# Kernel optimization log

Measured on AMD Instinct MI355X. Metric: run time of the kernel, lower is better.

## Reference

```python
import jax, jax.numpy as jnp
import numpy as np

NUM_CLASSES = 80
TOPK = 100
EPS = 1e-6


def _conv(x, w, b, pad):
    y = jax.lax.conv_general_dilated(
        x, w, window_strides=(1, 1), padding=[(pad, pad), (pad, pad)],
        dimension_numbers=('NCHW', 'OIHW', 'NCHW'))
    return y + b[None, :, None, None]


def _seek_local_maximum(p):
    # 8-neighbor local-maximum test with zero padding, plus >= EPS threshold.
    pp = jnp.pad(p, ((0, 0), (0, 0), (1, 1), (1, 1)))
    m = ((p >= pp[:, :, :-2, 1:-1]) & (p >= pp[:, :, 2:, 1:-1]) &
         (p >= pp[:, :, 1:-1, :-2]) & (p >= pp[:, :, 1:-1, 2:]) &
         (p >= pp[:, :, :-2, :-2]) & (p >= pp[:, :, :-2, 2:]) &
         (p >= pp[:, :, 2:, :-2]) & (p >= pp[:, :, 2:, 2:]) &
         (p >= EPS))
    return m.astype(p.dtype)


def setup_inputs() -> dict:
    key = jax.random.key(0)
    k = jax.random.split(key, 4)
    B, C, H, W = 8, 256, 128, 128
    return {
        'x': jax.random.normal(k[0], (B, C, H, W), jnp.float32),
        'pos_embeddings': jax.random.normal(k[1], (1, C, H, W), jnp.float32),
        'w1': jax.random.normal(k[2], (C, C, 3, 3), jnp.float32) * 0.02,
        'b1': jnp.zeros((C,), jnp.float32),
        'w2': jax.random.normal(k[3], (NUM_CLASSES + 1, C, 1, 1), jnp.float32) * 0.02,
        'b2': jnp.zeros((NUM_CLASSES + 1,), jnp.float32),
    }


def reference(x, pos_embeddings, w1, b1, w2, b2):
    b, c, h, w = x.shape
    # conv3x3 -> relu -> conv1x1 class logits  [b, num_classes+1, h, w]
    logits = _conv(jax.nn.relu(_conv(x, w1, b1, 1)), w2, b2, 0)
    probs = jax.nn.softmax(logits, axis=1)
    # keep only the winning foreground class per pixel (one-hot mask)
    cls_idx = jnp.argmax(probs[:, :NUM_CLASSES], axis=1)  # [b, h, w]
    one_hot = jax.nn.one_hot(cls_idx, NUM_CLASSES + 1, dtype=probs.dtype)
    probs = probs * jnp.transpose(one_hot, (0, 3, 1, 2))
    # boost local maxima (unrolled NMS) then topk over best-class score map
    probs = probs + _seek_local_maximum(probs)
    scores = jnp.max(probs[:, :NUM_CLASSES], axis=1).reshape(b, h * w)
    _, idx = jax.lax.top_k(scores, TOPK)  # [b, TOPK]
    topk_proposals = jnp.take_along_axis(
        x.reshape(b, c, h * w), idx[:, None, :], axis=2)
    pe = jnp.broadcast_to(pos_embeddings, (b,) + pos_embeddings.shape[1:])
    topk_pos_embeddings = jnp.take_along_axis(
        pe.reshape(b, -1, h * w), idx[:, None, :], axis=2)
    # eval mode: topk_locations is None in the original; omit it here
    return topk_proposals, topk_pos_embeddings, logits
```

## Files before the change

### kernel.cpp

```cpp
#include <hip/hip_runtime.h>
#include <cmath>

#define BATCH 8
#define CHN 256
#define HH 128
#define WW 128
#define HWSZ (HH*WW)
#define NCLS 81
#define NFG 80
#define KTOP 100
#define EPSV 1e-6f

typedef __attribute__((ext_vector_type(8))) short short8;
typedef __attribute__((ext_vector_type(4))) float f32x4;

__device__ __forceinline__ ushort f2bf(float f) {
    unsigned u = __float_as_uint(f);
    return (ushort)((u + 0x7FFFu + ((u >> 16) & 1u)) >> 16);
}
__device__ __forceinline__ float bf2f(ushort h) {
    return __uint_as_float(((unsigned)h) << 16);
}

__device__ __forceinline__ void gl16(const void* g, void* l) {
    __builtin_amdgcn_global_load_lds(
        (const __attribute__((address_space(1))) void*)g,
        (__attribute__((address_space(3))) void*)l, 16, 0, 0);
}

__global__ __launch_bounds__(256) void prep_x(
    const float* __restrict__ x, ushort* __restrict__ xh, ushort* __restrict__ xl)
{
    __shared__ float tile[32 * 321];
    const int blk = blockIdx.x;
    const int q4 = blk & 3, h = (blk >> 2) & 127, b = blk >> 9;
    const int w0 = q4 << 5;
    const int t = threadIdx.x;
    const int px1 = t & 31, cq = t >> 5;

    const float* xb = x + ((size_t)b * CHN) * HWSZ + h * WW + w0;
#pragma unroll 4
    for (int i = 0; i < 32; ++i) {
        tile[px1 * 321 + i * 10 + cq] = xb[(size_t)(i * 8 + cq) * HWSZ + px1];
    }
    __syncthreads();
    for (int i = 0; i < 4; ++i) {
        int u = i * 256 + t;
        int c8 = u & 31, px = u >> 5;
        short8 hv, lv;
#pragma unroll
        for (int j = 0; j < 8; ++j) {
            float f = tile[px * 321 + c8 * 10 + j];
            ushort hb = f2bf(f);
            hv[j] = (short)hb;
            lv[j] = (short)f2bf(f - bf2f(hb));
        }
        size_t addr = ((size_t)b * HWSZ + h * WW + w0 + px) * CHN + c8 * 8;
        *(short8*)(xh + addr) = hv;
        *(short8*)(xl + addr) = lv;
    }
}

__global__ __launch_bounds__(256) void prep_w(
    const float* __restrict__ w1, const float* __restrict__ w2,
    ushort* __restrict__ Bsw, ushort* __restrict__ w2sw)
{
    int i = blockIdx.x * 256 + threadIdx.x;
    if (i < 73728) {
        int tap  = i >> 13;
        int rem  = i & 8191;
        int kt   = rem >> 10;
        int rem2 = rem & 1023;
        int ntg  = rem2 >> 6;
        int lane = rem2 & 63;
        int oc   = ntg * 16 + (lane & 15);
        int ic0  = kt * 32 + (lane >> 4) * 8;
        size_t base = (size_t)(tap * 8 + kt) * 16384 + (size_t)ntg * 512 + lane * 8;
#pragma unroll
        for (int j = 0; j < 8; ++j) {
            float w  = w1[(size_t)oc * 2304 + (ic0 + j) * 9 + tap];
            ushort hb = f2bf(w);
            Bsw[base + j]        = hb;
            Bsw[base + 8192 + j] = f2bf(w - bf2f(hb));
        }
    } else {
        int j2 = i - 73728;
        int kt   = j2 / 768;
        int rem  = j2 - kt * 768;
        int spl  = rem / 384;
        int rem2 = rem - spl * 384;
        int ntg  = rem2 >> 6;
        int lane = rem2 & 63;
        int oc   = ntg * 16 + (lane & 15);
        int ic0  = kt * 32 + (lane >> 4) * 8;
        size_t base = (size_t)(kt * 12 + spl * 6 + ntg) * 512 + lane * 8;
#pragma unroll
        for (int j = 0; j < 8; ++j) {
            float w = (oc < NCLS) ? w2[(size_t)oc * CHN + ic0 + j] : 0.f;
            ushort hb = f2bf(w);
            w2sw[base + j] = spl ? f2bf(w - bf2f(hb)) : hb;
        }
    }
}

__global__ __launch_bounds__(256, 2) void conv3_pipe(
    const ushort* __restrict__ xh, const ushort* __restrict__ xl,
    const ushort* __restrict__ Bsw, const float* __restrict__ b1,
    float* __restrict__ y)
{
    __shared__ ushort A[3][2][132 * 32];

    const int blk  = blockIdx.x;
    const int b    = blk & 7;
    const int h    = blk >> 3;
    const int t    = threadIdx.x;
    const int lane = t & 63;
    const int w    = t >> 6;
    const int l15  = lane & 15;
    const int q    = lane >> 4;

    int colb[4], basew[4];
#pragma unroll
    for (int r = 0; r < 4; ++r) {
        int e   = (r * 256 + t) & 511;
        int pxs = (e >> 2) + 1;
        int qq  = e & 3;
        int qs  = qq ^ ((pxs >> 1) & 3);
        colb[r]  = (pxs - 1) * CHN + qs * 8;
        basew[r] = ((((r * 256 + (t & 192)) & 511) >> 2) + 1) * 32;
    }

    int abase[3];
#pragma unroll
    for (int kw = 0; kw < 3; ++kw) {
        int p0 = l15 + kw;
        abase[kw] = p0 * 64 + ((q ^ ((p0 >> 1) & 3)) << 4);
    }

    const short8 zz = {0, 0, 0, 0, 0, 0, 0, 0};
    f32x4 acc[8][4];
#pragma unroll
    for (int i = 0; i < 8; ++i)
#pragma unroll
        for (int j = 0; j < 4; ++j) { f32x4 z = {0.f, 0.f, 0.f, 0.f}; acc[i][j] = z; }

    if (t < 96) {
        int sl = t >> 5, rr = t & 31, arr = rr >> 4, pp = (rr >> 2) & 3, qq = rr & 3;
        int pxs = pp ? 128 + pp : 0;
        *(short8*)&A[sl][arr][pxs * 32 + qq * 8] = zz;
    }
    if (h == 0 || h == 127) {
        const int sl = (h == 0) ? 0 : 2;
        for (int u = t; u < 1056; u += 256) {
            int arr = u >= 528; int v = arr ? u - 528 : u;
            *(short8*)&A[sl][arr][v * 8] = zz;
        }
    }

    auto stage = [&](int sn) {
        int kt1 = sn / 3;
        int kh1 = sn - kt1 * 3;
        int gh  = h - 1 + kh1;
        if ((unsigned)gh < (unsigned)HH) {
            size_t rowb = ((size_t)(b * HH + gh) * WW) * CHN + kt1 * 32;
#pragma unroll
            for (int r = 0; r < 4; ++r) {
                const ushort* g = (r < 2 ? xh : xl) + rowb + colb[r];
                gl16(g, &A[kh1][r >> 1][basew[r]]);
            }
        }
    };

    stage(0);
    stage(1);

#pragma unroll 1
    for (int s = 0; s < 24; ++s) {
        const int kt = s / 3;
        const int kh = s - kt * 3;
        {
            const int kh1n = (s + 1) % 3;
            const bool nx4 = (s < 23) &&
                !((h == 0 && kh1n == 0) || (h == 127 && kh1n == 2));
            if (nx4) asm volatile("s_waitcnt vmcnt(4) lgkmcnt(0)" ::: "memory");
            else     asm volatile("s_waitcnt vmcnt(0) lgkmcnt(0)" ::: "memory");
            __builtin_amdgcn_s_barrier();
            __builtin_amdgcn_sched_barrier(0);
        }
#pragma unroll
        for (int kw = 0; kw < 3; ++kw) {
            const int tap = kh * 3 + kw;
            const char* bkh = (const char*)Bsw +
                ((size_t)(tap * 8 + kt) << 15) + (w << 12) + (lane << 4);
            const char* bkl = bkh + 16384;
            short8 bh[4], bl[4];
#pragma unroll
            for (int nt = 0; nt < 4; ++nt) {
                bh[nt] = *(const short8*)(bkh + nt * 1024);
                bl[nt] = *(const short8*)(bkl + nt * 1024);
            }
            if (kw == 0 && s < 22) stage(s + 2);
            const char* pah = (const char*)&A[kh][0][0] + abase[kw];
            const char* pal = (const char*)&A[kh][1][0] + abase[kw];
#pragma unroll
            for (int mth = 0; mth < 8; mth += 4) {
                short8 ahf[4], alf[4];
#pragma unroll
                for (int mm = 0; mm < 4; ++mm) {
                    ahf[mm] = *(const short8*)(pah + (mth + mm) * 1024);
                    alf[mm] = *(const short8*)(pal + (mth + mm) * 1024);
                }
                __builtin_amdgcn_s_setprio(1);
#pragma unroll
                for (int nt = 0; nt < 4; ++nt) {
#pragma unroll
                    for (int mm = 0; mm < 4; ++mm)
                        acc[mth + mm][nt] = __builtin_amdgcn_mfma_f32_16x16x32_bf16(
                            ahf[mm], bh[nt], acc[mth + mm][nt], 0, 0, 0);
#pragma unroll
                    for (int mm = 0; mm < 4; ++mm)
                        acc[mth + mm][nt] = __builtin_amdgcn_mfma_f32_16x16x32_bf16(
                            ahf[mm], bl[nt], acc[mth + mm][nt], 0, 0, 0);
#pragma unroll
                    for (int mm = 0; mm < 4; ++mm)
                        acc[mth + mm][nt] = __builtin_amdgcn_mfma_f32_16x16x32_bf16(
                            alf[mm], bh[nt], acc[mth + mm][nt], 0, 0, 0);
                }
                __builtin_amdgcn_s_setprio(0);
            }
        }
    }

    const size_t rowbase = (size_t)b * HWSZ + h * WW;
#pragma unroll
    for (int nt = 0; nt < 4; ++nt) {
        const int oc = w * 64 + nt * 16 + l15;
        const float bias = b1[oc];
#pragma unroll
        for (int mt = 0; mt < 8; ++mt) {
#pragma unroll
            for (int r = 0; r < 4; ++r) {
                const int px = mt * 16 + q * 4 + r;
                float v = acc[mt][nt][r] + bias;
                y[(rowbase + px) * CHN + oc] = v > 0.f ? v : 0.f;
            }
        }
    }
}

__global__ __launch_bounds__(256) void head_mfma(
    const float* __restrict__ y, const ushort* __restrict__ w2sw,
    const float* __restrict__ b2, float* __restrict__ logits_out,
    int* __restrict__ cls_map, float* __restrict__ prob_map)
{
    __shared__ float ls[128][97];
    const int blk = blockIdx.x;
    const int b = blk >> 7, h = blk & 127;
    const int t = threadIdx.x, lane = t & 63, wm = t >> 6;
    const int l15 = lane & 15, q = lane >> 4;

    f32x4 acc[2][6];
#pragma unroll
    for (int i = 0; i < 2; ++i)
#pragma unroll
        for (int j = 0; j < 6; ++j) { f32x4 z = {0.f, 0.f, 0.f, 0.f}; acc[i][j] = z; }

    const size_t rowbase = (size_t)b * HWSZ + h * WW;
    const float* yb0 = y + (rowbase + wm * 32 + l15) * CHN + q * 8;
    const float* yb1 = yb0 + 16 * CHN;

    float4 fa[2][4], fb[2][4];
#pragma unroll
    for (int k = 0; k < 4; ++k) {
        fa[0][k] = *(const float4*)(yb0 + k * 32);
        fb[0][k] = *(const float4*)(yb0 + k * 32 + 4);
        fa[1][k] = *(const float4*)(yb1 + k * 32);
        fb[1][k] = *(const float4*)(yb1 + k * 32 + 4);
    }

#pragma unroll
    for (int kt = 0; kt < 8; ++kt) {
        const int sl = kt & 3;
        short8 ah[2], al[2];
#pragma unroll
        for (int mt = 0; mt < 2; ++mt) {
            float4 f0 = fa[mt][sl];
            float4 f1 = fb[mt][sl];
            float fv[8] = {f0.x, f0.y, f0.z, f0.w, f1.x, f1.y, f1.z, f1.w};
#pragma unroll
            for (int j = 0; j < 8; ++j) {
                ushort hb = f2bf(fv[j]);
                ah[mt][j] = (short)hb;
                al[mt][j] = (short)f2bf(fv[j] - bf2f(hb));
            }
        }
        if (kt < 4) {
            fa[0][sl] = *(const float4*)(yb0 + (kt + 4) * 32);
            fb[0][sl] = *(const float4*)(yb0 + (kt + 4) * 32 + 4);
            fa[1][sl] = *(const float4*)(yb1 + (kt + 4) * 32);
            fb[1][sl] = *(const float4*)(yb1 + (kt + 4) * 32 + 4);
        }
        const ushort* bk = w2sw + (size_t)kt * 12 * 512 + lane * 8;
#pragma unroll
        for (int nt = 0; nt < 6; ++nt) {
            short8 bh = *(const short8*)(bk + nt * 512);
            short8 bl = *(const short8*)(bk + (6 + nt) * 512);
#pragma unroll
            for (int mt = 0; mt < 2; ++mt) {
                acc[mt][nt] = __builtin_amdgcn_mfma_f32_16x16x32_bf16(ah[mt], bh, acc[mt][nt], 0, 0, 0);
                acc[mt][nt] = __builtin_amdgcn_mfma_f32_16x16x32_bf16(ah[mt], bl, acc[mt][nt], 0, 0, 0);
                acc[mt][nt] = __builtin_amdgcn_mfma_f32_16x16x32_bf16(al[mt], bh, acc[mt][nt], 0, 0, 0);
            }
        }
    }

#pragma unroll
    for (int nt = 0; nt < 6; ++nt) {
        const int oc = nt * 16 + l15;
        const float bias = (oc < NCLS) ? b2[oc] : 0.f;
#pragma unroll
        for (int mt = 0; mt < 2; ++mt) {
#pragma unroll
            for (int r = 0; r < 4; ++r) {
                const int px = wm * 32 + mt * 16 + q * 4 + r;
                ls[px][oc] = acc[mt][nt][r] + bias;
            }
        }
    }
    __syncthreads();

    for (int i = t; i < NCLS * 128; i += 256) {
        int c = i >> 7, px = i & 127;
        logits_out[((size_t)b * NCLS + c) * HWSZ + h * WW + px] = ls[px][c];
    }

    if (t < 128) {
        const int px = t;
        float m = -1e30f;
#pragma unroll
        for (int c = 0; c < NCLS; ++c) m = fmaxf(m, ls[px][c]);
        float s = 0.f;
        for (int c = 0; c < NCLS; ++c) s += expf(ls[px][c] - m);
        float best = -1e30f; int bc = 0;
        for (int c = 0; c < NFG; ++c) {
            float v = ls[px][c];
            if (v > best) { best = v; bc = c; }
        }
        cls_map[rowbase + px]  = bc;
        prob_map[rowbase + px] = expf(best - m) / s;
    }
}

__global__ __launch_bounds__(256) void locmax_kernel(
    const int* __restrict__ cls_map, const float* __restrict__ prob_map,
    float* __restrict__ score)
{
    int i = blockIdx.x * 256 + threadIdx.x;
    int b = i >> 14;
    int p = i & (HWSZ - 1);
    int h = p >> 7, w = p & 127;
    int mycls = cls_map[i];
    float myp = prob_map[i];
    bool lm = (myp >= EPSV);
#pragma unroll
    for (int dh = -1; dh <= 1; ++dh)
#pragma unroll
        for (int dw = -1; dw <= 1; ++dw) {
            if (dh == 0 && dw == 0) continue;
            int nh = h + dh, nw = w + dw;
            if ((unsigned)nh < HH && (unsigned)nw < WW) {
                int ni = b * HWSZ + nh * WW + nw;
                if (cls_map[ni] == mycls && myp < prob_map[ni]) lm = false;
            }
        }
    score[i] = myp + (lm ? 1.f : 0.f);
}

__global__ __launch_bounds__(1024) void topk_kernel(
    const float* __restrict__ score, int* __restrict__ idx_out)
{
    __shared__ unsigned int hist[256];
    __shared__ unsigned int suf[256];
    __shared__ unsigned long long cand[2048];
    __shared__ unsigned int sprefix, sneed, scntA, scntB;
    const int b = blockIdx.x;
    const int t = threadIdx.x;
    const float* sc = score + b * HWSZ;

    unsigned keys[16];
#pragma unroll
    for (int i = 0; i < 16; ++i)
        keys[i] = __float_as_uint(sc[t + (i << 10)]);

    if (t == 0) { sneed = KTOP; sprefix = 0; scntA = 0; scntB = 0; }

    for (int lvl = 0; lvl < 4; ++lvl) {
        const int shift = 24 - 8 * lvl;
        if (t < 256) hist[t] = 0;
        __syncthreads();
        const unsigned pref = sprefix;
#pragma unroll
        for (int i = 0; i < 16; ++i) {
            unsigned k = keys[i];
            bool match = (lvl == 0) || ((k >> (shift + 8)) == pref);
            if (match) atomicAdd(&hist[(k >> shift) & 255u], 1u);
        }
        __syncthreads();
        if (t < 256) suf[t] = hist[t];
        __syncthreads();
#pragma unroll
        for (int st = 1; st < 256; st <<= 1) {
            unsigned v = 0;
            if (t < 256 && t + st < 256) v = suf[t + st];
            __syncthreads();
            if (t < 256) suf[t] += v;
            __syncthreads();
        }
        const unsigned needv = sneed;
        __syncthreads();
        if (t < 256) {
            unsigned sj  = suf[t];
            unsigned sj1 = (t == 255) ? 0u : suf[t + 1];
            if (sj >= needv && sj1 < needv) {
                sprefix = (pref << 8) | (unsigned)t;
                sneed   = needv - sj1;
            }
        }
        __syncthreads();
    }

    const unsigned K = sprefix;
#pragma unroll
    for (int i = 0; i < 16; ++i) {
        unsigned k = keys[i];
        int p = t + (i << 10);
        if (k > K) {
            unsigned pos = atomicAdd(&scntA, 1u);
            cand[pos] = ((unsigned long long)k << 32) | (unsigned)(~p);
        } else if (k == K) {
            unsigned pos = atomicAdd(&scntB, 1u);
            if (pos < 1920u)
                cand[128 + pos] = ((unsigned long long)k << 32) | (unsigned)(~p);
        }
    }
    __syncthreads();
    const int cA = (int)scntA;
    const int cB = (int)(scntB < 1920u ? scntB : 1920u);
    const int Ctot = cA + cB;
    for (int ti = t; ti < Ctot; ti += 1024) {
        unsigned long long my = cand[ti < cA ? ti : 128 + (ti - cA)];
        int rank = 0;
        for (int j = 0; j < Ctot; ++j) {
            unsigned long long o = cand[j < cA ? j : 128 + (j - cA)];
            rank += (o > my) ? 1 : 0;
        }
        if (rank < KTOP)
            idx_out[b * KTOP + rank] =
                (int)(~(unsigned)(my & 0xFFFFFFFFull)) & (HWSZ - 1);
    }
}

__global__ __launch_bounds__(128) void gather_kernel(
    const float* __restrict__ x, const float* __restrict__ pos,
    const int* __restrict__ idx, float* __restrict__ out0,
    float* __restrict__ out1)
{
    int blk = blockIdx.x;
    int b = blk >> 8, c = blk & 255;
    int j = threadIdx.x;
    if (j < KTOP) {
        int pix = idx[b * KTOP + j];
        out0[((size_t)b * CHN + c) * KTOP + j] = x[((size_t)b * CHN + c) * HWSZ + pix];
        out1[((size_t)b * CHN + c) * KTOP + j] = pos[(size_t)c * HWSZ + pix];
    }
}

extern "C" void kernel_launch(void* const* d_in, const int* in_sizes, int n_in,
                              void* d_out, int out_size, void* d_ws, size_t ws_size,
                              hipStream_t stream) {
    (void)in_sizes; (void)n_in; (void)out_size; (void)ws_size;
    const float* x   = (const float*)d_in[0];
    const float* pos = (const float*)d_in[1];
    const float* w1  = (const float*)d_in[2];
    const float* b1  = (const float*)d_in[3];
    const float* w2  = (const float*)d_in[4];
    const float* b2  = (const float*)d_in[5];

    float* out0   = (float*)d_out;
    float* out1   = out0 + BATCH * CHN * KTOP;
    float* logits = out1 + BATCH * CHN * KTOP;

    char* ws = (char*)d_ws;
    const size_t NPX = (size_t)BATCH * HWSZ;

    size_t off = 0;
    int*    cls_map  = (int*)(ws + off);    off += NPX * 4;
    float*  prob_map = (float*)(ws + off);  off += NPX * 4;
    float*  score    = (float*)(ws + off);  off += NPX * 4;
    int*    idx      = (int*)(ws + off);    off += 4096;
    ushort* w2sw     = (ushort*)(ws + off); off += (size_t)8 * 12 * 512 * 2;
    ushort* Bsw      = (ushort*)(ws + off); off += (size_t)9 * 8 * 16384 * 2;
    ushort* xh       = (ushort*)(ws + off); off += NPX * CHN * 2;
    ushort* xl       = (ushort*)(ws + off); off += NPX * CHN * 2;
    float*  y        = (float*)(ws + off);  off += NPX * CHN * 4;

    prep_x<<<4096, 256, 0, stream>>>(x, xh, xl);
    prep_w<<<312, 256, 0, stream>>>(w1, w2, Bsw, w2sw);
    conv3_pipe<<<1024, 256, 0, stream>>>(xh, xl, Bsw, b1, y);
    head_mfma<<<1024, 256, 0, stream>>>(y, w2sw, b2, logits, cls_map, prob_map);
    locmax_kernel<<<(int)(NPX / 256), 256, 0, stream>>>(cls_map, prob_map, score);
    topk_kernel<<<BATCH, 1024, 0, stream>>>(score, idx);
    gather_kernel<<<BATCH * CHN, 128, 0, stream>>>(x, pos, idx, out0, out1);
}
```

Baseline: 664.4 us.

## Switch conv3x3 MFMA from 16x16x32 to 32x32x16 bf16 tiles

Changes the conv3x3 kernel's inner product from 16x16x32 MFMA instructions to 32x32x16 ones. It reorganizes the weight swizzle in prep_w, the LDS A-fragment addressing and the accumulator layout to match. The larger tiles mean fewer LDS fragment loads per FLOP and fewer MFMA issues, which should raise matrix-core utilisation. The epilogue's pixel-index mapping is rewritten for the 32x32 output layout, so any mistake there would show up as a correctness bug.

```diff
diff --git a/kernel.cpp b/kernel.cpp
--- a/kernel.cpp
+++ b/kernel.cpp
@@ -13,6 +13,7 @@
 
 typedef __attribute__((ext_vector_type(8))) short short8;
 typedef __attribute__((ext_vector_type(4))) float f32x4;
+typedef __attribute__((ext_vector_type(16))) float f32x16;
 
 __device__ __forceinline__ ushort f2bf(float f) {
     unsigned u = __float_as_uint(f);
@@ -71,11 +72,14 @@
         int rem  = i & 8191;
         int kt   = rem >> 10;
         int rem2 = rem & 1023;
-        int ntg  = rem2 >> 6;
+        int fgrp = rem2 >> 6;
         int lane = rem2 & 63;
-        int oc   = ntg * 16 + (lane & 15);
-        int ic0  = kt * 32 + (lane >> 4) * 8;
-        size_t base = (size_t)(tap * 8 + kt) * 16384 + (size_t)ntg * 512 + lane * 8;
+        int wv   = fgrp >> 2;
+        int n    = (fgrp >> 1) & 1;
+        int ks   = fgrp & 1;
+        int oc   = wv * 64 + n * 32 + (lane & 31);
+        int ic0  = kt * 32 + ks * 16 + (lane >> 5) * 8;
+        size_t base = (size_t)(tap * 8 + kt) * 16384 + (size_t)fgrp * 512 + lane * 8;
 #pragma unroll
         for (int j = 0; j < 8; ++j) {
             float w  = w1[(size_t)oc * 2304 + (ic0 + j) * 9 + tap];
@@ -116,8 +120,8 @@
     const int t    = threadIdx.x;
     const int lane = t & 63;
     const int w    = t >> 6;
-    const int l15  = lane & 15;
-    const int q    = lane >> 4;
+    const int la   = lane & 31;
+    const int g    = lane >> 5;
 
     int colb[4], basew[4];
 #pragma unroll
@@ -130,19 +134,24 @@
         basew[r] = ((((r * 256 + (t & 192)) & 511) >> 2) + 1) * 32;
     }
 
-    int abase[3];
+    int abks[3][2];
 #pragma unroll
     for (int kw = 0; kw < 3; ++kw) {
-        int p0 = l15 + kw;
-        abase[kw] = p0 * 64 + ((q ^ ((p0 >> 1) & 3)) << 4);
+        int la2 = la + kw;
+        int sw  = (la2 >> 1) & 3;
+#pragma unroll
+        for (int ks = 0; ks < 2; ++ks)
+            abks[kw][ks] = la2 * 64 + (((((ks << 1) | g)) ^ sw) << 4);
     }
 
     const short8 zz = {0, 0, 0, 0, 0, 0, 0, 0};
-    f32x4 acc[8][4];
-#pragma unroll
-    for (int i = 0; i < 8; ++i)
-#pragma unroll
-        for (int j = 0; j < 4; ++j) { f32x4 z = {0.f, 0.f, 0.f, 0.f}; acc[i][j] = z; }
+    f32x16 acc[4][2];
+#pragma unroll
+    for (int i = 0; i < 4; ++i)
+#pragma unroll
+        for (int j = 0; j < 2; ++j)
+#pragma unroll
+            for (int r = 0; r < 16; ++r) acc[i][j][r] = 0.f;
 
     if (t < 96) {
         int sl = t >> 5, rr = t & 31, arr = rr >> 4, pp = (rr >> 2) & 3, qq = rr & 3;
@@ -165,8 +174,8 @@
             size_t rowb = ((size_t)(b * HH + gh) * WW) * CHN + kt1 * 32;
 #pragma unroll
             for (int r = 0; r < 4; ++r) {
-                const ushort* g = (r < 2 ? xh : xl) + rowb + colb[r];
-                gl16(g, &A[kh1][r >> 1][basew[r]]);
+                const ushort* gp = (r < 2 ? xh : xl) + rowb + colb[r];
+                gl16(gp, &A[kh1][r >> 1][basew[r]]);
             }
         }
     };
@@ -193,39 +202,44 @@
             const char* bkh = (const char*)Bsw +
                 ((size_t)(tap * 8 + kt) << 15) + (w << 12) + (lane << 4);
             const char* bkl = bkh + 16384;
-            short8 bh[4], bl[4];
-#pragma unroll
-            for (int nt = 0; nt < 4; ++nt) {
-                bh[nt] = *(const short8*)(bkh + nt * 1024);
-                bl[nt] = *(const short8*)(bkl + nt * 1024);
-            }
+            short8 bh[2][2], bl[2][2];
+#pragma unroll
+            for (int n = 0; n < 2; ++n)
+#pragma unroll
+                for (int ks = 0; ks < 2; ++ks) {
+                    bh[n][ks] = *(const short8*)(bkh + (n * 2 + ks) * 1024);
+                    bl[n][ks] = *(const short8*)(bkl + (n * 2 + ks) * 1024);
+                }
             if (kw == 0 && s < 22) stage(s + 2);
-            const char* pah = (const char*)&A[kh][0][0] + abase[kw];
-            const char* pal = (const char*)&A[kh][1][0] + abase[kw];
-#pragma unroll
-            for (int mth = 0; mth < 8; mth += 4) {
-                short8 ahf[4], alf[4];
-#pragma unroll
-                for (int mm = 0; mm < 4; ++mm) {
-                    ahf[mm] = *(const short8*)(pah + (mth + mm) * 1024);
-                    alf[mm] = *(const short8*)(pal + (mth + mm) * 1024);
+            const char* pah = (const char*)&A[kh][0][0];
+            const char* pal = (const char*)&A[kh][1][0];
+#pragma unroll
+            for (int ks = 0; ks < 2; ++ks) {
+                short8 ah[4], al[4];
+#pragma unroll
+                for (int m = 0; m < 4; ++m) {
+                    ah[m] = *(const short8*)(pah + abks[kw][ks] + m * 2048);
+                    al[m] = *(const short8*)(pal + abks[kw][ks] + m * 2048);
                 }
                 __builtin_amdgcn_s_setprio(1);
 #pragma unroll
-                for (int nt = 0; nt < 4; ++nt) {
-#pragma unroll
-                    for (int mm = 0; mm < 4; ++mm)
-                        acc[mth + mm][nt] = __builtin_amdgcn_mfma_f32_16x16x32_bf16(
-                            ahf[mm], bh[nt], acc[mth + mm][nt], 0, 0, 0);
-#pragma unroll
-                    for (int mm = 0; mm < 4; ++mm)
-                        acc[mth + mm][nt] = __builtin_amdgcn_mfma_f32_16x16x32_bf16(
-                            ahf[mm], bl[nt], acc[mth + mm][nt], 0, 0, 0);
-#pragma unroll
-                    for (int mm = 0; mm < 4; ++mm)
-                        acc[mth + mm][nt] = __builtin_amdgcn_mfma_f32_16x16x32_bf16(
-                            alf[mm], bh[nt], acc[mth + mm][nt], 0, 0, 0);
-                }
+                for (int n = 0; n < 2; ++n)
+#pragma unroll
+                    for (int m = 0; m < 4; ++m)
+                        acc[m][n] = __builtin_amdgcn_mfma_f32_32x32x16_bf16(
+                            ah[m], bh[n][ks], acc[m][n], 0, 0, 0);
+#pragma unroll
+                for (int n = 0; n < 2; ++n)
+#pragma unroll
+                    for (int m = 0; m < 4; ++m)
+                        acc[m][n] = __builtin_amdgcn_mfma_f32_32x32x16_bf16(
+                            ah[m], bl[n][ks], acc[m][n], 0, 0, 0);
+#pragma unroll
+                for (int n = 0; n < 2; ++n)
+#pragma unroll
+                    for (int m = 0; m < 4; ++m)
+                        acc[m][n] = __builtin_amdgcn_mfma_f32_32x32x16_bf16(
+                            al[m], bh[n][ks], acc[m][n], 0, 0, 0);
                 __builtin_amdgcn_s_setprio(0);
             }
         }
@@ -233,15 +247,15 @@
 
     const size_t rowbase = (size_t)b * HWSZ + h * WW;
 #pragma unroll
-    for (int nt = 0; nt < 4; ++nt) {
-        const int oc = w * 64 + nt * 16 + l15;
+    for (int n = 0; n < 2; ++n) {
+        const int oc = w * 64 + n * 32 + la;
         const float bias = b1[oc];
 #pragma unroll
-        for (int mt = 0; mt < 8; ++mt) {
-#pragma unroll
-            for (int r = 0; r < 4; ++r) {
-                const int px = mt * 16 + q * 4 + r;
-                float v = acc[mt][nt][r] + bias;
+        for (int m = 0; m < 4; ++m) {
+#pragma unroll
+            for (int reg = 0; reg < 16; ++reg) {
+                const int px = m * 32 + (reg & 3) + 8 * (reg >> 2) + 4 * g;
+                float v = acc[m][n][reg] + bias;
                 y[(rowbase + px) * CHN + oc] = v > 0.f ? v : 0.f;
             }
         }
```

New measurement: 706.2 us. 6.3% more time.

## Split conv3x3 row tile into half-width blocks for higher occupancy

Applied to the files above, without the earlier changes.

The 3x3 conv kernel now processes 64 pixels of a row per block instead of 128, doubling the grid to 2048 blocks and halving both the accumulator register tile and the LDS staging buffer (with halo columns loaded separately). Launch bounds are raised to 3 blocks per SM to hide latency with more resident waves. In exchange, each B-weight fragment loaded from global memory is reused over half as many MFMAs, doubling weight traffic, and halo loads add some overhead.

```diff
diff --git a/kernel.cpp b/kernel.cpp
--- a/kernel.cpp
+++ b/kernel.cpp
@@ -103,32 +103,34 @@
     }
 }
 
-__global__ __launch_bounds__(256, 2) void conv3_pipe(
+__global__ __launch_bounds__(256, 3) void conv3_occ(
     const ushort* __restrict__ xh, const ushort* __restrict__ xl,
     const ushort* __restrict__ Bsw, const float* __restrict__ b1,
     float* __restrict__ y)
 {
-    __shared__ ushort A[3][2][132 * 32];
+    __shared__ ushort A[3][2][68 * 32];
 
     const int blk  = blockIdx.x;
     const int b    = blk & 7;
-    const int h    = blk >> 3;
+    const int h    = (blk >> 3) & 127;
+    const int ws2  = blk >> 10;
+    const int w0   = ws2 << 6;
     const int t    = threadIdx.x;
     const int lane = t & 63;
-    const int w    = t >> 6;
+    const int wv   = t >> 6;
     const int l15  = lane & 15;
     const int q    = lane >> 4;
 
-    int colb[4], basew[4];
-#pragma unroll
-    for (int r = 0; r < 4; ++r) {
-        int e   = (r * 256 + t) & 511;
-        int pxs = (e >> 2) + 1;
-        int qq  = e & 3;
-        int qs  = qq ^ ((pxs >> 1) & 3);
-        colb[r]  = (pxs - 1) * CHN + qs * 8;
-        basew[r] = ((((r * 256 + (t & 192)) & 511) >> 2) + 1) * 32;
-    }
+    const int mrow = 1 + wv * 16 + (lane >> 2);
+    const int mqs  = (lane & 3) ^ ((mrow >> 1) & 3);
+    const int mcol = (w0 + wv * 16 + (lane >> 2)) * CHN + mqs * 8;
+    const int mdst = (1 + wv * 16) * 32;
+    const int hrow = ws2 ? 0 : 65;
+    const int hgw  = w0 - 1 + hrow;
+    const int ha   = wv >> 1;
+    const int hqb  = (wv & 1) * 2;
+    const int hcol = hgw * CHN + (hqb + (lane & 1)) * 8;
+    const int hdst = hrow * 32 + hqb * 8;
 
     int abase[3];
 #pragma unroll
@@ -138,22 +140,22 @@
     }
 
     const short8 zz = {0, 0, 0, 0, 0, 0, 0, 0};
-    f32x4 acc[8][4];
-#pragma unroll
-    for (int i = 0; i < 8; ++i)
+    f32x4 acc[4][4];
+#pragma unroll
+    for (int i = 0; i < 4; ++i)
 #pragma unroll
         for (int j = 0; j < 4; ++j) { f32x4 z = {0.f, 0.f, 0.f, 0.f}; acc[i][j] = z; }
 
-    if (t < 96) {
-        int sl = t >> 5, rr = t & 31, arr = rr >> 4, pp = (rr >> 2) & 3, qq = rr & 3;
-        int pxs = pp ? 128 + pp : 0;
-        *(short8*)&A[sl][arr][pxs * 32 + qq * 8] = zz;
+    if (t < 24) {
+        int sl = t >> 3, rr = t & 7, a = rr >> 2, qq = rr & 3;
+        int zrow = ws2 ? 65 : 0;
+        *(short8*)&A[sl][a][zrow * 32 + qq * 8] = zz;
     }
     if (h == 0 || h == 127) {
         const int sl = (h == 0) ? 0 : 2;
-        for (int u = t; u < 1056; u += 256) {
-            int arr = u >= 528; int v = arr ? u - 528 : u;
-            *(short8*)&A[sl][arr][v * 8] = zz;
+        for (int u = t; u < 544; u += 256) {
+            int a = u >= 272; int v = a ? u - 272 : u;
+            *(short8*)&A[sl][a][v * 8] = zz;
         }
     }
 
@@ -163,11 +165,10 @@
         int gh  = h - 1 + kh1;
         if ((unsigned)gh < (unsigned)HH) {
             size_t rowb = ((size_t)(b * HH + gh) * WW) * CHN + kt1 * 32;
-#pragma unroll
-            for (int r = 0; r < 4; ++r) {
-                const ushort* g = (r < 2 ? xh : xl) + rowb + colb[r];
-                gl16(g, &A[kh1][r >> 1][basew[r]]);
-            }
+            gl16(xh + rowb + mcol, &A[kh1][0][mdst]);
+            gl16(xl + rowb + mcol, &A[kh1][1][mdst]);
+            if (lane < 2)
+                gl16((ha ? xl : xh) + rowb + hcol, &A[kh1][ha][hdst]);
         }
     };
 
@@ -180,10 +181,10 @@
         const int kh = s - kt * 3;
         {
             const int kh1n = (s + 1) % 3;
-            const bool nx4 = (s < 23) &&
+            const bool nx = (s < 23) &&
                 !((h == 0 && kh1n == 0) || (h == 127 && kh1n == 2));
-            if (nx4) asm volatile("s_waitcnt vmcnt(4) lgkmcnt(0)" ::: "memory");
-            else     asm volatile("s_waitcnt vmcnt(0) lgkmcnt(0)" ::: "memory");
+            if (nx) asm volatile("s_waitcnt vmcnt(3) lgkmcnt(0)" ::: "memory");
+            else    asm volatile("s_waitcnt vmcnt(0) lgkmcnt(0)" ::: "memory");
             __builtin_amdgcn_s_barrier();
             __builtin_amdgcn_sched_barrier(0);
         }
@@ -191,7 +192,7 @@
         for (int kw = 0; kw < 3; ++kw) {
             const int tap = kh * 3 + kw;
             const char* bkh = (const char*)Bsw +
-                ((size_t)(tap * 8 + kt) << 15) + (w << 12) + (lane << 4);
+                ((size_t)(tap * 8 + kt) << 15) + (wv << 12) + (lane << 4);
             const char* bkl = bkh + 16384;
             short8 bh[4], bl[4];
 #pragma unroll
@@ -201,43 +202,43 @@
             }
             if (kw == 0 && s < 22) stage(s + 2);
             const char* pah = (const char*)&A[kh][0][0] + abase[kw];
-            const char* pal = (const char*)&A[kh][1][0] + abase[kw];
-#pragma unroll
-            for (int mth = 0; mth < 8; mth += 4) {
-                short8 ahf[4], alf[4];
-#pragma unroll
-                for (int mm = 0; mm < 4; ++mm) {
-                    ahf[mm] = *(const short8*)(pah + (mth + mm) * 1024);
-                    alf[mm] = *(const short8*)(pal + (mth + mm) * 1024);
-                }
-                __builtin_amdgcn_s_setprio(1);
-#pragma unroll
-                for (int nt = 0; nt < 4; ++nt) {
-#pragma unroll
-                    for (int mm = 0; mm < 4; ++mm)
-                        acc[mth + mm][nt] = __builtin_amdgcn_mfma_f32_16x16x32_bf16(
-                            ahf[mm], bh[nt], acc[mth + mm][nt], 0, 0, 0);
-#pragma unroll
-                    for (int mm = 0; mm < 4; ++mm)
-                        acc[mth + mm][nt] = __builtin_amdgcn_mfma_f32_16x16x32_bf16(
-                            ahf[mm], bl[nt], acc[mth + mm][nt], 0, 0, 0);
-#pragma unroll
-                    for (int mm = 0; mm < 4; ++mm)
-                        acc[mth + mm][nt] = __builtin_amdgcn_mfma_f32_16x16x32_bf16(
-                            alf[mm], bh[nt], acc[mth + mm][nt], 0, 0, 0);
-                }
-                __builtin_amdgcn_s_setprio(0);
-            }
-        }
-    }
-
-    const size_t rowbase = (size_t)b * HWSZ + h * WW;
+            const char* pal = pah + 4352;
+            short8 ahf[4], alf[4];
+#pragma unroll
+            for (int mm = 0; mm < 4; ++mm) {
+                ahf[mm] = *(const short8*)(pah + mm * 1024);
+                alf[mm] = *(const short8*)(pal + mm * 1024);
+            }
+            __builtin_amdgcn_s_setprio(1);
+#pragma unroll
+            for (int nt = 0; nt < 4; ++nt)
+#pragma unroll
+                for (int mm = 0; mm < 4; ++mm)
+                    acc[mm][nt] = __builtin_amdgcn_mfma_f32_16x16x32_bf16(
+                        ahf[mm], bh[nt], acc[mm][nt], 0, 0, 0);
+#pragma unroll
+            for (int nt = 0; nt < 4; ++nt)
+#pragma unroll
+                for (int mm = 0; mm < 4; ++mm)
+                    acc[mm][nt] = __builtin_amdgcn_mfma_f32_16x16x32_bf16(
+                        ahf[mm], bl[nt], acc[mm][nt], 0, 0, 0);
+#pragma unroll
+            for (int nt = 0; nt < 4; ++nt)
+#pragma unroll
+                for (int mm = 0; mm < 4; ++mm)
+                    acc[mm][nt] = __builtin_amdgcn_mfma_f32_16x16x32_bf16(
+                        alf[mm], bh[nt], acc[mm][nt], 0, 0, 0);
+            __builtin_amdgcn_s_setprio(0);
+        }
+    }
+
+    const size_t rowbase = (size_t)b * HWSZ + h * WW + w0;
 #pragma unroll
     for (int nt = 0; nt < 4; ++nt) {
-        const int oc = w * 64 + nt * 16 + l15;
+        const int oc = wv * 64 + nt * 16 + l15;
         const float bias = b1[oc];
 #pragma unroll
-        for (int mt = 0; mt < 8; ++mt) {
+        for (int mt = 0; mt < 4; ++mt) {
 #pragma unroll
             for (int r = 0; r < 4; ++r) {
                 const int px = mt * 16 + q * 4 + r;
@@ -506,7 +507,7 @@
 
     prep_x<<<4096, 256, 0, stream>>>(x, xh, xl);
     prep_w<<<312, 256, 0, stream>>>(w1, w2, Bsw, w2sw);
-    conv3_pipe<<<1024, 256, 0, stream>>>(xh, xl, Bsw, b1, y);
+    conv3_occ<<<2048, 256, 0, stream>>>(xh, xl, Bsw, b1, y);
     head_mfma<<<1024, 256, 0, stream>>>(y, w2sw, b2, logits, cls_map, prob_map);
     locmax_kernel<<<(int)(NPX / 256), 256, 0, stream>>>(cls_map, prob_map, score);
     topk_kernel<<<BATCH, 1024, 0, stream>>>(score, idx);
```

New measurement: 689.4 us. 3.8% more time.

## Fuse prep kernels and merge locmax, topk and gather into one kernel

Applied to the files above, without the earlier changes.

Combines the two preprocessing kernels into a single launch split by block index. It also folds the local-maximum scoring and the final gather into the per-batch top-k kernel, keeping the selected indices in shared memory. This removes three kernel launches and the score and index round-trips through global memory. In exchange, the locmax and gather work now runs on only 8 blocks instead of many, so parallelism for those phases drops sharply.

```diff
diff --git a/kernel.cpp b/kernel.cpp
--- a/kernel.cpp
+++ b/kernel.cpp
@@ -28,77 +28,77 @@
         (__attribute__((address_space(3))) void*)l, 16, 0, 0);
 }
 
-__global__ __launch_bounds__(256) void prep_x(
-    const float* __restrict__ x, ushort* __restrict__ xh, ushort* __restrict__ xl)
+__global__ __launch_bounds__(256) void prep_all(
+    const float* __restrict__ x, ushort* __restrict__ xh, ushort* __restrict__ xl,
+    const float* __restrict__ w1, const float* __restrict__ w2,
+    ushort* __restrict__ Bsw, ushort* __restrict__ w2sw)
 {
     __shared__ float tile[32 * 321];
     const int blk = blockIdx.x;
-    const int q4 = blk & 3, h = (blk >> 2) & 127, b = blk >> 9;
-    const int w0 = q4 << 5;
     const int t = threadIdx.x;
-    const int px1 = t & 31, cq = t >> 5;
-
-    const float* xb = x + ((size_t)b * CHN) * HWSZ + h * WW + w0;
+
+    if (blk < 4096) {
+        const int q4 = blk & 3, h = (blk >> 2) & 127, b = blk >> 9;
+        const int w0 = q4 << 5;
+        const int px1 = t & 31, cq = t >> 5;
+
+        const float* xb = x + ((size_t)b * CHN) * HWSZ + h * WW + w0;
 #pragma unroll 4
-    for (int i = 0; i < 32; ++i) {
-        tile[px1 * 321 + i * 10 + cq] = xb[(size_t)(i * 8 + cq) * HWSZ + px1];
-    }
-    __syncthreads();
-    for (int i = 0; i < 4; ++i) {
-        int u = i * 256 + t;
-        int c8 = u & 31, px = u >> 5;
-        short8 hv, lv;
-#pragma unroll
-        for (int j = 0; j < 8; ++j) {
-            float f = tile[px * 321 + c8 * 10 + j];
-            ushort hb = f2bf(f);
-            hv[j] = (short)hb;
-            lv[j] = (short)f2bf(f - bf2f(hb));
-        }
-        size_t addr = ((size_t)b * HWSZ + h * WW + w0 + px) * CHN + c8 * 8;
-        *(short8*)(xh + addr) = hv;
-        *(short8*)(xl + addr) = lv;
-    }
-}
-
-__global__ __launch_bounds__(256) void prep_w(
-    const float* __restrict__ w1, const float* __restrict__ w2,
-    ushort* __restrict__ Bsw, ushort* __restrict__ w2sw)
-{
-    int i = blockIdx.x * 256 + threadIdx.x;
-    if (i < 73728) {
-        int tap  = i >> 13;
-        int rem  = i & 8191;
-        int kt   = rem >> 10;
-        int rem2 = rem & 1023;
-        int ntg  = rem2 >> 6;
-        int lane = rem2 & 63;
-        int oc   = ntg * 16 + (lane & 15);
-        int ic0  = kt * 32 + (lane >> 4) * 8;
-        size_t base = (size_t)(tap * 8 + kt) * 16384 + (size_t)ntg * 512 + lane * 8;
-#pragma unroll
-        for (int j = 0; j < 8; ++j) {
-            float w  = w1[(size_t)oc * 2304 + (ic0 + j) * 9 + tap];
-            ushort hb = f2bf(w);
-            Bsw[base + j]        = hb;
-            Bsw[base + 8192 + j] = f2bf(w - bf2f(hb));
+        for (int i = 0; i < 32; ++i) {
+            tile[px1 * 321 + i * 10 + cq] = xb[(size_t)(i * 8 + cq) * HWSZ + px1];
+        }
+        __syncthreads();
+        for (int i = 0; i < 4; ++i) {
+            int u = i * 256 + t;
+            int c8 = u & 31, px = u >> 5;
+            short8 hv, lv;
+#pragma unroll
+            for (int j = 0; j < 8; ++j) {
+                float f = tile[px * 321 + c8 * 10 + j];
+                ushort hb = f2bf(f);
+                hv[j] = (short)hb;
+                lv[j] = (short)f2bf(f - bf2f(hb));
+            }
+            size_t addr = ((size_t)b * HWSZ + h * WW + w0 + px) * CHN + c8 * 8;
+            *(short8*)(xh + addr) = hv;
+            *(short8*)(xl + addr) = lv;
         }
     } else {
-        int j2 = i - 73728;
-        int kt   = j2 / 768;
-        int rem  = j2 - kt * 768;
-        int spl  = rem / 384;
-        int rem2 = rem - spl * 384;
-        int ntg  = rem2 >> 6;
-        int lane = rem2 & 63;
-        int oc   = ntg * 16 + (lane & 15);
-        int ic0  = kt * 32 + (lane >> 4) * 8;
-        size_t base = (size_t)(kt * 12 + spl * 6 + ntg) * 512 + lane * 8;
-#pragma unroll
-        for (int j = 0; j < 8; ++j) {
-            float w = (oc < NCLS) ? w2[(size_t)oc * CHN + ic0 + j] : 0.f;
-            ushort hb = f2bf(w);
-            w2sw[base + j] = spl ? f2bf(w - bf2f(hb)) : hb;
+        int i = (blk - 4096) * 256 + t;
+        if (i < 73728) {
+            int tap  = i >> 13;
+            int rem  = i & 8191;
+            int kt   = rem >> 10;
+            int rem2 = rem & 1023;
+            int ntg  = rem2 >> 6;
+            int lane = rem2 & 63;
+            int oc   = ntg * 16 + (lane & 15);
+            int ic0  = kt * 32 + (lane >> 4) * 8;
+            size_t base = (size_t)(tap * 8 + kt) * 16384 + (size_t)ntg * 512 + lane * 8;
+#pragma unroll
+            for (int j = 0; j < 8; ++j) {
+                float w  = w1[(size_t)oc * 2304 + (ic0 + j) * 9 + tap];
+                ushort hb = f2bf(w);
+                Bsw[base + j]        = hb;
+                Bsw[base + 8192 + j] = f2bf(w - bf2f(hb));
+            }
+        } else {
+            int j2 = i - 73728;
+            int kt   = j2 / 768;
+            int rem  = j2 - kt * 768;
+            int spl  = rem / 384;
+            int rem2 = rem - spl * 384;
+            int ntg  = rem2 >> 6;
+            int lane = rem2 & 63;
+            int oc   = ntg * 16 + (lane & 15);
+            int ic0  = kt * 32 + (lane >> 4) * 8;
+            size_t base = (size_t)(kt * 12 + spl * 6 + ntg) * 512 + lane * 8;
+#pragma unroll
+            for (int j = 0; j < 8; ++j) {
+                float w = (oc < NCLS) ? w2[(size_t)oc * CHN + ic0 + j] : 0.f;
+                ushort hb = f2bf(w);
+                w2sw[base + j] = spl ? f2bf(w - bf2f(hb)) : hb;
+            }
         }
     }
 }
@@ -351,46 +351,41 @@
     }
 }
 
-__global__ __launch_bounds__(256) void locmax_kernel(
+__global__ __launch_bounds__(1024) void topk_fused(
     const int* __restrict__ cls_map, const float* __restrict__ prob_map,
-    float* __restrict__ score)
-{
-    int i = blockIdx.x * 256 + threadIdx.x;
-    int b = i >> 14;
-    int p = i & (HWSZ - 1);
-    int h = p >> 7, w = p & 127;
-    int mycls = cls_map[i];
-    float myp = prob_map[i];
-    bool lm = (myp >= EPSV);
-#pragma unroll
-    for (int dh = -1; dh <= 1; ++dh)
-#pragma unroll
-        for (int dw = -1; dw <= 1; ++dw) {
-            if (dh == 0 && dw == 0) continue;
-            int nh = h + dh, nw = w + dw;
-            if ((unsigned)nh < HH && (unsigned)nw < WW) {
-                int ni = b * HWSZ + nh * WW + nw;
-                if (cls_map[ni] == mycls && myp < prob_map[ni]) lm = false;
-            }
-        }
-    score[i] = myp + (lm ? 1.f : 0.f);
-}
-
-__global__ __launch_bounds__(1024) void topk_kernel(
-    const float* __restrict__ score, int* __restrict__ idx_out)
+    const float* __restrict__ x, const float* __restrict__ pos,
+    float* __restrict__ out0, float* __restrict__ out1)
 {
     __shared__ unsigned int hist[256];
     __shared__ unsigned int suf[256];
     __shared__ unsigned long long cand[2048];
+    __shared__ int sidx[KTOP];
     __shared__ unsigned int sprefix, sneed, scntA, scntB;
     const int b = blockIdx.x;
     const int t = threadIdx.x;
-    const float* sc = score + b * HWSZ;
+    const int base = b * HWSZ;
 
     unsigned keys[16];
 #pragma unroll
-    for (int i = 0; i < 16; ++i)
-        keys[i] = __float_as_uint(sc[t + (i << 10)]);
+    for (int i = 0; i < 16; ++i) {
+        const int p = t + (i << 10);
+        const int h = p >> 7, w = p & 127;
+        const int mycls = cls_map[base + p];
+        const float myp = prob_map[base + p];
+        bool lm = (myp >= EPSV);
+#pragma unroll
+        for (int dh = -1; dh <= 1; ++dh)
+#pragma unroll
+            for (int dw = -1; dw <= 1; ++dw) {
+                if (dh == 0 && dw == 0) continue;
+                int nh = h + dh, nw = w + dw;
+                if ((unsigned)nh < HH && (unsigned)nw < WW) {
+                    int ni = base + nh * WW + nw;
+                    if (cls_map[ni] == mycls && myp < prob_map[ni]) lm = false;
+                }
+            }
+        keys[i] = __float_as_uint(myp + (lm ? 1.f : 0.f));
+    }
 
     if (t == 0) { sneed = KTOP; sprefix = 0; scntA = 0; scntB = 0; }
 
@@ -435,12 +430,12 @@
         unsigned k = keys[i];
         int p = t + (i << 10);
         if (k > K) {
-            unsigned pos = atomicAdd(&scntA, 1u);
-            cand[pos] = ((unsigned long long)k << 32) | (unsigned)(~p);
+            unsigned pos2 = atomicAdd(&scntA, 1u);
+            cand[pos2] = ((unsigned long long)k << 32) | (unsigned)(~p);
         } else if (k == K) {
-            unsigned pos = atomicAdd(&scntB, 1u);
-            if (pos < 1920u)
-                cand[128 + pos] = ((unsigned long long)k << 32) | (unsigned)(~p);
+            unsigned pos2 = atomicAdd(&scntB, 1u);
+            if (pos2 < 1920u)
+                cand[128 + pos2] = ((unsigned long long)k << 32) | (unsigned)(~p);
         }
     }
     __syncthreads();
@@ -455,21 +450,13 @@
             rank += (o > my) ? 1 : 0;
         }
         if (rank < KTOP)
-            idx_out[b * KTOP + rank] =
-                (int)(~(unsigned)(my & 0xFFFFFFFFull)) & (HWSZ - 1);
-    }
-}
-
-__global__ __launch_bounds__(128) void gather_kernel(
-    const float* __restrict__ x, const float* __restrict__ pos,
-    const int* __restrict__ idx, float* __restrict__ out0,
-    float* __restrict__ out1)
-{
-    int blk = blockIdx.x;
-    int b = blk >> 8, c = blk & 255;
-    int j = threadIdx.x;
-    if (j < KTOP) {
-        int pix = idx[b * KTOP + j];
+            sidx[rank] = (int)(~(unsigned)(my & 0xFFFFFFFFull)) & (HWSZ - 1);
+    }
+    __syncthreads();
+
+    for (int u = t; u < CHN * KTOP; u += 1024) {
+        int c = u / KTOP, j = u - c * KTOP;
+        int pix = sidx[j];
         out0[((size_t)b * CHN + c) * KTOP + j] = x[((size_t)b * CHN + c) * HWSZ + pix];
         out1[((size_t)b * CHN + c) * KTOP + j] = pos[(size_t)c * HWSZ + pix];
     }
@@ -496,19 +483,14 @@
     size_t off = 0;
     int*    cls_map  = (int*)(ws + off);    off += NPX * 4;
     float*  prob_map = (float*)(ws + off);  off += NPX * 4;
-    float*  score    = (float*)(ws + off);  off += NPX * 4;
-    int*    idx      = (int*)(ws + off);    off += 4096;
     ushort* w2sw     = (ushort*)(ws + off); off += (size_t)8 * 12 * 512 * 2;
     ushort* Bsw      = (ushort*)(ws + off); off += (size_t)9 * 8 * 16384 * 2;
     ushort* xh       = (ushort*)(ws + off); off += NPX * CHN * 2;
     ushort* xl       = (ushort*)(ws + off); off += NPX * CHN * 2;
     float*  y        = (float*)(ws + off);  off += NPX * CHN * 4;
 
-    prep_x<<<4096, 256, 0, stream>>>(x, xh, xl);
-    prep_w<<<312, 256, 0, stream>>>(w1, w2, Bsw, w2sw);
+    prep_all<<<4408, 256, 0, stream>>>(x, xh, xl, w1, w2, Bsw, w2sw);
     conv3_pipe<<<1024, 256, 0, stream>>>(xh, xl, Bsw, b1, y);
     head_mfma<<<1024, 256, 0, stream>>>(y, w2sw, b2, logits, cls_map, prob_map);
-    locmax_kernel<<<(int)(NPX / 256), 256, 0, stream>>>(cls_map, prob_map, score);
-    topk_kernel<<<BATCH, 1024, 0, stream>>>(score, idx);
-    gather_kernel<<<BATCH * CHN, 128, 0, stream>>>(x, pos, idx, out0, out1);
-}
+    topk_fused<<<BATCH, 1024, 0, stream>>>(cls_map, prob_map, x, pos, out0, out1);
+}
```

Measured after the change: 796.1 us. 1.2x slower.
